# Kernel optimization log

Hardware: AMD Instinct MI355X
Metric: run time of the kernel (lower is better)

## Reference

```python
import jax, jax.numpy as jnp
import numpy as np

B, S, D, CH = 4, 2048, 1024, 64
MEM_LR, MEM_MOM, MEM_DECAY = 0.1, 0.9, 0.01
EPS = 1.1920929e-07  # torch RMSNorm default eps (float32 finfo eps)


def setup_inputs() -> dict:
    key = jax.random.key(0)
    ks = jax.random.split(key, 20)
    rn = lambda i, shape, s: jax.random.normal(ks[i], shape, dtype=jnp.float32) * s
    inp = {
        "x": jax.random.normal(ks[0], (B, S, D), dtype=jnp.float32),
        # archetypal metric M = I + small perturbation (near-identity, as in ArchetypalProjection)
        "Mmet": jnp.eye(D, dtype=jnp.float32)[None, :, :] + rn(1, (B, D, D), 0.02),
        # projections (bias-free, xavier-ish scale)
        "Wk": rn(2, (D, D), 0.02), "Wv": rn(3, (D, D), 0.02),
        "Wq": rn(4, (D, D), 0.02), "Wo": rn(5, (D, D), 0.02),
        # gate Linears (with bias) for decay / lr / momentum
        "Wgd": rn(6, (D, D), 0.02), "bgd": rn(7, (D,), 0.02),
        "Wgl": rn(8, (D, D), 0.02), "bgl": rn(9, (D,), 0.02),
        "Wgm": rn(10, (D, D), 0.02), "bgm": rn(11, (D,), 0.02),
        # RMSNorm gains
        "g_store": jnp.ones((D,), dtype=jnp.float32),
        "g_retr": jnp.ones((D,), dtype=jnp.float32),
        # memory MLP initial weights (depth=2, std=0.02)
        "W0": rn(12, (D, D), 0.02), "W1": rn(13, (D, D), 0.02),
    }
    return inp


def rmsnorm(x, g):
    return x * jax.lax.rsqrt(jnp.mean(x * x, axis=-1, keepdims=True) + EPS) * g


def l2norm(x):
    n = jnp.linalg.norm(x, axis=-1, keepdims=True)
    return x / jnp.maximum(n, 1e-12)


def mem_fwd(h, W0, W1):
    # 2-layer bias-free MLP with SiLU between layers (MemoryMLP, depth=2)
    return jax.nn.silu(h @ W0.T) @ W1.T


def forward(x, Mmet, Wk, Wv, Wq, Wo, Wgd, bgd, Wgl, bgl, Wgm, bgm, g_store, g_retr, W0, W1):
    Bs, Ss, Ds = x.shape
    pad = (-Ss) % CH
    xp = jnp.pad(x, ((0, 0), (0, pad), (0, 0))) if pad else x
    N = xp.shape[1] // CH

    # data-dependent per-chunk gates from chunk means -> batch-averaged scalars [N]
    cm = xp.reshape(Bs, N, CH, Ds).mean(axis=2)            # [B,N,D]
    alpha = jax.nn.sigmoid(cm @ Wgd.T + bgd).mean(-1).mean(0) * MEM_DECAY  # [N]
    theta = jax.nn.sigmoid(cm @ Wgl.T + bgl).mean(-1).mean(0) * MEM_LR     # [N]
    eta = jax.nn.sigmoid(cm @ Wgm.T + bgm).mean(-1).mean(0) * MEM_MOM      # [N]

    # store path: RMSNorm -> curved-space keys via archetypal metric
    xs = rmsnorm(xp, g_store)
    k = l2norm(jax.nn.silu(jnp.einsum('bsd,bde->bse', xs, Mmet) @ Wk.T))
    v = jax.nn.silu(xs @ Wv.T)
    # retrieve path
    q = l2norm(jax.nn.silu(rmsnorm(xp, g_retr) @ Wq.T))

    to_chunks = lambda t: t.reshape(Bs, N, CH, Ds).transpose(1, 0, 2, 3)  # [N,B,C,D]
    kc, vc, qc = to_chunks(k), to_chunks(v), to_chunks(q)

    def assoc_loss(params, kk, vv):
        return jnp.mean((mem_fwd(kk, *params) - vv) ** 2)

    grad_fn = jax.grad(assoc_loss)

    def step(carry, inp):
        W0c, W1c, S0, S1 = carry
        qt, kt, vt, a, th, et = inp
        r = mem_fwd(qt, W0c, W1c)                 # retrieve BEFORE update (causal)
        g0, g1 = grad_fn((W0c, W1c), kt, vt)      # surprise gradient
        S0n = et * S0 - th * g0                   # Eq. 14
        S1n = et * S1 - th * g1
        W0n = (1.0 - a) * W0c + S0n               # Eq. 13
        W1n = (1.0 - a) * W1c + S1n
        return (W0n, W1n, S0n, S1n), r

    init = (W0, W1, jnp.zeros_like(W0), jnp.zeros_like(W1))
    _, ret = jax.lax.scan(step, init, (qc, kc, vc, alpha, theta, eta))  # ret: [N,B,C,D]
    out = ret.transpose(1, 0, 2, 3).reshape(Bs, N * CH, Ds)[:, :Ss, :] @ Wo.T
    return out


def reference(x, Mmet, Wk, Wv, Wq, Wo, Wgd, bgd, Wgl, bgl, Wgm, bgm, g_store, g_retr, W0, W1):
    return forward(x, Mmet, Wk, Wv, Wq, Wo, Wgd, bgd, Wgl, bgl, Wgm, bgm, g_store, g_retr, W0, W1)
```

## Files before the change

### kernel.cpp

```cpp
#include <hip/hip_runtime.h>
#include <math.h>

static constexpr int B_ = 4, S_ = 2048, D_ = 1024, CH_ = 64, N_ = 32;
static constexpr float EPS_ = 1.1920929e-07f;
static constexpr float C2_  = 2.0f / 262144.0f;
static constexpr int GRID_ = 128;

typedef __attribute__((ext_vector_type(8))) short bf16x8;
typedef __attribute__((ext_vector_type(4))) short bf16x4;
typedef __attribute__((ext_vector_type(4))) float f32x4;

__device__ __forceinline__ float sigf(float x)  { return 1.f/(1.f+expf(-x)); }
__device__ __forceinline__ float siluf(float x) { return x/(1.f+expf(-x)); }
__device__ __forceinline__ float silugrad(float x){
  float s = 1.f/(1.f+expf(-x));
  return s*(1.f + x*(1.f-s));
}
__device__ __forceinline__ short f2b(float f){
  union{float f;unsigned u;}c; c.f=f;
  unsigned u=c.u;
  return (short)((u + 0x7fffu + ((u>>16)&1u)) >> 16);
}
__device__ __forceinline__ float b2f(short h){
  union{unsigned u;float f;}c; c.u=((unsigned)(unsigned short)h)<<16; return c.f;
}

template<int LPS>
__device__ __forceinline__ void wait_vm(int c){
  if (c <= 0)      asm volatile("s_waitcnt vmcnt(0)" ::: "memory");
  else if (c == 1) asm volatile("s_waitcnt vmcnt(%0)" :: "i"(LPS)   : "memory");
  else             asm volatile("s_waitcnt vmcnt(%0)" :: "i"(2*LPS) : "memory");
}

template<int MT, int NT, int DEPTH>
__device__ __forceinline__ void score(
    const short* __restrict__ A, const short* __restrict__ Bm,
    int K, int lda, int ldb, int bm0, int bn0, short* stg,
    f32x4 (&acc)[MT/32][NT/32])
{
  constexpr int MF = MT/32, NF = NT/32;
  constexpr int ACH = MT*8, BCH = NT*8, T = 256;
  constexpr int BUF = (MT+NT)*64;
  constexpr int LPS = (ACH+BCH)/T;
  const int tid = threadIdx.x, lane = tid & 63, w = tid >> 6;
  const int wm = w>>1, wn = w&1, lrow = lane & 15, lk8 = lane >> 4;

  #pragma unroll
  for (int i=0;i<MF;++i)
    #pragma unroll
    for (int j=0;j<NF;++j) acc[i][j] = (f32x4){0.f,0.f,0.f,0.f};

  auto stage = [&](int s){
    short* la = stg + (s & (DEPTH-1))*BUF;
    short* lb = la + MT*64;
    const int k0 = s*64;
    #pragma unroll
    for (int i=tid; i<ACH; i+=T){
      int row = i>>3, sc = (i&7) ^ (row&7);
      const short* src = A + (size_t)(bm0+row)*lda + k0 + (sc<<3);
      __builtin_amdgcn_global_load_lds(
        (const __attribute__((address_space(1))) void*)src,
        (__attribute__((address_space(3))) void*)(la + i*8), 16, 0, 0);
    }
    #pragma unroll
    for (int i=tid; i<BCH; i+=T){
      int row = i>>3, sc = (i&7) ^ (row&7);
      const short* src = Bm + (size_t)(bn0+row)*ldb + k0 + (sc<<3);
      __builtin_amdgcn_global_load_lds(
        (const __attribute__((address_space(1))) void*)src,
        (__attribute__((address_space(3))) void*)(lb + i*8), 16, 0, 0);
    }
  };

  const int nk = K >> 6;
  for (int s=0; s<DEPTH-1 && s<nk; ++s) stage(s);
  for (int ks=0; ks<nk; ++ks){
    int C = nk - ks; if (C > DEPTH-1) C = DEPTH-1;
    wait_vm<LPS>(C-1);
    __builtin_amdgcn_s_barrier();
    __builtin_amdgcn_sched_barrier(0);
    if (ks + DEPTH-1 < nk) stage(ks + DEPTH-1);
    short* la = stg + (ks & (DEPTH-1))*BUF;
    short* lb = la + MT*64;
    #pragma unroll
    for (int kk=0; kk<2; ++kk){
      bf16x8 af[MF], bfr[NF];
      #pragma unroll
      for (int mi=0;mi<MF;++mi){
        int row = wm*(MT/2) + mi*16 + lrow;
        int ch = row*8 + ((kk*4+lk8) ^ (row&7));
        af[mi] = *(const bf16x8*)(la + ch*8);
      }
      #pragma unroll
      for (int ni=0;ni<NF;++ni){
        int row = wn*(NT/2) + ni*16 + lrow;
        int ch = row*8 + ((kk*4+lk8) ^ (row&7));
        bfr[ni] = *(const bf16x8*)(lb + ch*8);
      }
      #pragma unroll
      for (int mi=0;mi<MF;++mi)
        #pragma unroll
        for (int ni=0;ni<NF;++ni)
          acc[mi][ni] = __builtin_amdgcn_mfma_f32_16x16x32_bf16(af[mi], bfr[ni], acc[mi][ni], 0,0,0);
    }
  }
}

template<int WMW, int WNW, int DEPTH, class Epi>
__device__ __forceinline__ void gemm_core(
    const short* __restrict__ A, const short* __restrict__ Bm,
    int K, int lda, int ldb, int bm0, int bn0, short* lds, Epi epi)
{
  constexpr int BK = 64, CPR = 8;
  constexpr int BMR = WMW*64, BNR = WNW*64, T = WMW*WNW*64;
  constexpr int ACH = BMR*CPR, BCH = BNR*CPR;
  constexpr int BUF = (BMR+BNR)*BK;
  constexpr int LPS = (ACH+BCH)/T;
  const int tid = threadIdx.x, lane = tid & 63, w = tid >> 6;
  const int wm = w / WNW, wn = w % WNW, lrow = lane & 15, lk8 = lane >> 4;

  f32x4 acc[4][4];
  #pragma unroll
  for (int i=0;i<4;++i)
    #pragma unroll
    for (int j=0;j<4;++j) acc[i][j] = (f32x4){0.f,0.f,0.f,0.f};

  auto stage = [&](int s){
    short* la = lds + (s & (DEPTH-1))*BUF;
    short* lb = la + BMR*BK;
    const int k0 = s*BK;
    #pragma unroll
    for (int i=tid; i<ACH; i+=T){
      int row = i>>3, sc = (i&7) ^ (row&7);
      const short* src = A + (size_t)(bm0+row)*lda + k0 + (sc<<3);
      __builtin_amdgcn_global_load_lds(
        (const __attribute__((address_space(1))) void*)src,
        (__attribute__((address_space(3))) void*)(la + i*8), 16, 0, 0);
    }
    #pragma unroll
    for (int i=tid; i<BCH; i+=T){
      int row = i>>3, sc = (i&7) ^ (row&7);
      const short* src = Bm + (size_t)(bn0+row)*ldb + k0 + (sc<<3);
      __builtin_amdgcn_global_load_lds(
        (const __attribute__((address_space(1))) void*)src,
        (__attribute__((address_space(3))) void*)(lb + i*8), 16, 0, 0);
    }
  };

  const int nk = K >> 6;
  for (int s=0; s<DEPTH-1 && s<nk; ++s) stage(s);
  for (int ks=0; ks<nk; ++ks){
    int C = nk - ks; if (C > DEPTH-1) C = DEPTH-1;
    wait_vm<LPS>(C-1);
    __builtin_amdgcn_s_barrier();
    __builtin_amdgcn_sched_barrier(0);
    if (ks + DEPTH-1 < nk) stage(ks + DEPTH-1);
    short* la = lds + (ks & (DEPTH-1))*BUF;
    short* lb = la + BMR*BK;
    #pragma unroll
    for (int kk=0; kk<2; ++kk){
      bf16x8 af[4], bfr[4];
      #pragma unroll
      for (int mi=0;mi<4;++mi){
        int row = wm*64 + mi*16 + lrow;
        int ch = row*8 + ((kk*4+lk8) ^ (row&7));
        af[mi] = *(const bf16x8*)(la + ch*8);
      }
      #pragma unroll
      for (int ni=0;ni<4;++ni){
        int row = wn*64 + ni*16 + lrow;
        int ch = row*8 + ((kk*4+lk8) ^ (row&7));
        bfr[ni] = *(const bf16x8*)(lb + ch*8);
      }
      #pragma unroll
      for (int mi=0;mi<4;++mi)
        #pragma unroll
        for (int ni=0;ni<4;++ni)
          acc[mi][ni] = __builtin_amdgcn_mfma_f32_16x16x32_bf16(af[mi], bfr[ni], acc[mi][ni], 0,0,0);
    }
  }
  #pragma unroll
  for (int mi=0;mi<4;++mi)
    #pragma unroll
    for (int ni=0;ni<4;++ni)
      epi(bm0 + wm*64 + mi*16 + lk8*4, bn0 + wn*64 + ni*16 + lrow, acc[mi][ni]);
}

struct EpiOut { float* C;
  __device__ void operator()(int r0,int c,f32x4 q) const {
    #pragma unroll
    for (int j=0;j<4;++j) C[(size_t)(r0+j)*D_+c]=q[j]; } };

struct EpiStoreBf { short* C;
  __device__ void operator()(int r0,int c,f32x4 q) const {
    #pragma unroll
    for (int j=0;j<4;++j) C[(size_t)(r0+j)*D_+c]=f2b(q[j]); } };

struct EpiBiasSig { float* C; const float* bias;
  __device__ void operator()(int r0,int c,f32x4 q) const {
    #pragma unroll
    for (int j=0;j<4;++j) C[(size_t)(r0+j)*D_+c] = sigf(q[j] + bias[c]); } };

struct EpiScat { short* dst; int part;
  __device__ void operator()(int r0,int c,f32x4 q) const {
    #pragma unroll
    for (int j=0;j<4;++j){
      int r = r0+j;
      int b = r >> 11, s = r & 2047, t = s >> 6, ch = s & 63;
      short sv = f2b(siluf(q[j]));
      if (part < 0) dst[((size_t)t*256 +             b*64 + ch)*D_ + c] = sv;
      else          dst[((size_t)t*512 + part*256 + b*64 + ch)*D_ + c] = sv;
    } } };

template<int WMW, int WNW, class Epi>
__global__ __launch_bounds__(WMW*WNW*64)
void mgemm(const short* __restrict__ A, const short* __restrict__ Bm,
           int K, int lda, int ldb, Epi epi){
  __shared__ __align__(16) short lds[2*(WMW+WNW)*64*64];
  gemm_core<WMW,WNW,2>(A, Bm, K, lda, ldb, blockIdx.y*WMW*64, blockIdx.x*WNW*64, lds, epi);
}

__device__ __forceinline__ void gsync(int* cnt, int target){
  asm volatile("s_waitcnt vmcnt(0) lgkmcnt(0)" ::: "memory");
  __syncthreads();
  if (threadIdx.x == 0){
    __builtin_amdgcn_fence(__ATOMIC_RELEASE, "agent");
    __hip_atomic_fetch_add(cnt, 1, __ATOMIC_RELAXED, __HIP_MEMORY_SCOPE_AGENT);
    while (__hip_atomic_load(cnt, __ATOMIC_RELAXED, __HIP_MEMORY_SCOPE_AGENT) < target)
      __builtin_amdgcn_s_sleep(4);
    __builtin_amdgcn_fence(__ATOMIC_ACQUIRE, "agent");
  }
  __syncthreads();
}

__global__ __launch_bounds__(256)
void scan_coop(const short* __restrict__ qk, const short* __restrict__ vbuf,
               const short* __restrict__ ktT, const float* __restrict__ gates,
               short* __restrict__ preout, short* __restrict__ sgT,
               short* __restrict__ abuf, short* __restrict__ akT,
               short* __restrict__ dpred, short* __restrict__ dpredT, short* __restrict__ dh1T,
               const float* __restrict__ W0f, const float* __restrict__ W1f,
               short* __restrict__ W0b, short* __restrict__ W1b,
               short* __restrict__ W1bT0, short* __restrict__ W1bT1,
               int* __restrict__ bar)
{
  __shared__ __align__(16) float wM[128*132];
  __shared__ __align__(16) short stg[32768];
  const int bid = blockIdx.x;
  const int tid = threadIdx.x, lane = tid & 63, w = tid >> 6;
  const int wm = w>>1, wn = w&1, lrow = lane & 15, lk8 = lane >> 4;
  int* cnt = bar;
  int ep = 0;

  const bool ownW1 = bid < 64;
  const int ob = ownW1 ? bid : bid - 64;
  const int obm = (ob>>3)<<7, obn = (ob&7)<<7;
  const float* Wsrc = ownW1 ? W1f : W0f;
  for (int i=tid; i<4096; i+=256){
    int cl = i>>5, r4 = (i&31)<<2;
    f32x4 v = *(const f32x4*)&Wsrc[(size_t)(obn+cl)*D_ + obm + r4];
    *(f32x4*)&wM[cl*132 + r4] = v;
  }
  f32x4 sReg[4][4];
  #pragma unroll
  for (int i=0;i<4;++i)
    #pragma unroll
    for (int j=0;j<4;++j) sReg[i][j] = (f32x4){0.f,0.f,0.f,0.f};
  __syncthreads();

  const int pbm0 = (bid>>4)<<6, pbn0 = (bid&15)<<6;

  for (int t=0; t<N_; ++t){
    const short* qkt = qk + (size_t)t*512*D_;
    const float al = gates[t], th = gates[N_+t], et = gates[2*N_+t];
    short* W1Tcur = (t&1) ? W1bT1 : W1bT0;
    short* W1Tnxt = (t&1) ? W1bT0 : W1bT1;

    {
      f32x4 acc[2][2];
      score<64,64,4>(qkt, W0b, 1024, 1024, 1024, pbm0, pbn0, stg, acc);
      #pragma unroll
      for (int mi=0;mi<2;++mi)
        #pragma unroll
        for (int ni=0;ni<2;++ni){
          int r0 = pbm0 + wm*32 + mi*16 + lk8*4;
          int c  = pbn0 + wn*32 + ni*16 + lrow;
          f32x4 q = acc[mi][ni];
          bf16x4 a4, g4;
          #pragma unroll
          for (int j=0;j<4;++j){
            a4[j] = f2b(siluf(q[j]));
            g4[j] = f2b(silugrad(q[j]));
            abuf[(size_t)(r0+j)*D_+c] = a4[j];
          }
          if (r0 >= 256){ int rr = r0-256;
            *(bf16x4*)&akT[(size_t)c*256+rr] = a4;
            *(bf16x4*)&sgT[(size_t)c*256+rr] = g4; }
        }
    }
    gsync(cnt, (++ep)*GRID_);

    {
      const short* vt = vbuf + (size_t)t*256*D_;
      f32x4 acc[2][2];
      score<64,64,4>(abuf, W1b, 1024, 1024, 1024, pbm0, pbn0, stg, acc);
      #pragma unroll
      for (int mi=0;mi<2;++mi)
        #pragma unroll
        for (int ni=0;ni<2;++ni){
          int r0 = pbm0 + wm*32 + mi*16 + lk8*4;
          int c  = pbn0 + wn*32 + ni*16 + lrow;
          f32x4 q = acc[mi][ni];
          if (r0 < 256){
            #pragma unroll
            for (int j=0;j<4;++j){ int r=r0+j, b=r>>6, ch=r&63;
              preout[((size_t)b*S_ + t*CH_ + ch)*D_ + c] = f2b(q[j]); }
          } else { int rr = r0-256;
            bf16x4 d4;
            #pragma unroll
            for (int j=0;j<4;++j){
              float dv = C2_*(q[j] - b2f(vt[(size_t)(rr+j)*D_+c]));
              d4[j] = f2b(dv);
              dpred[(size_t)(rr+j)*D_+c] = d4[j];
            }
            *(bf16x4*)&dpredT[(size_t)c*256+rr] = d4; }
        }
    }
    gsync(cnt, (++ep)*GRID_);
    if (t == N_-1) break;

    if (ownW1){
      f32x4 acc[4][4];
      score<128,128,2>(akT, dpredT, 256, 256, 256, obm, obn, stg, acc);
      #pragma unroll
      for (int mi=0;mi<4;++mi)
        #pragma unroll
        for (int ni=0;ni<4;++ni){
          int rl = wm*64 + mi*16 + lk8*4;
          int cl = wn*64 + ni*16 + lrow;
          f32x4 w4 = *(f32x4*)&wM[cl*132 + rl];
          f32x4 s4 = sReg[mi][ni];
          bf16x4 nb;
          #pragma unroll
          for (int j=0;j<4;++j){
            float sv = et*s4[j] - th*acc[mi][ni][j];
            s4[j] = sv;
            float wv = (1.f-al)*w4[j] + sv;
            w4[j] = wv; nb[j] = f2b(wv);
          }
          sReg[mi][ni] = s4;
          *(f32x4*)&wM[cl*132 + rl] = w4;
          int r0 = obm + rl, c = obn + cl;
          *(bf16x4*)&W1b[(size_t)c*D_ + r0] = nb;
          #pragma unroll
          for (int j=0;j<4;++j) W1Tnxt[(size_t)(r0+j)*D_ + c] = nb[j];
        }
    } else {
      int b = bid - 64;
      int bm0 = (b&15)<<6, bn0 = (b>>4)<<6;
      f32x4 acc[2][2];
      score<64,64,4>(W1Tcur, dpred, 1024, 1024, 1024, bm0, bn0, stg, acc);
      #pragma unroll
      for (int mi=0;mi<2;++mi)
        #pragma unroll
        for (int ni=0;ni<2;++ni){
          int r0 = bm0 + wm*32 + mi*16 + lk8*4;
          int c  = bn0 + wn*32 + ni*16 + lrow;
          #pragma unroll
          for (int j=0;j<4;++j){
            size_t i = (size_t)(r0+j)*256 + c;
            dh1T[i] = f2b(acc[mi][ni][j] * b2f(sgT[i]));
          }
        }
    }
    gsync(cnt, (++ep)*GRID_);

    if (!ownW1){
      f32x4 acc[4][4];
      score<128,128,2>(ktT + (size_t)t*D_*256, dh1T, 256, 256, 256, obm, obn, stg, acc);
      #pragma unroll
      for (int mi=0;mi<4;++mi)
        #pragma unroll
        for (int ni=0;ni<4;++ni){
          int rl = wm*64 + mi*16 + lk8*4;
          int cl = wn*64 + ni*16 + lrow;
          f32x4 w4 = *(f32x4*)&wM[cl*132 + rl];
          f32x4 s4 = sReg[mi][ni];
          bf16x4 nb;
          #pragma unroll
          for (int j=0;j<4;++j){
            float sv = et*s4[j] - th*acc[mi][ni][j];
            s4[j] = sv;
            float wv = (1.f-al)*w4[j] + sv;
            w4[j] = wv; nb[j] = f2b(wv);
          }
          sReg[mi][ni] = s4;
          *(f32x4*)&wM[cl*132 + rl] = w4;
          int r0 = obm + rl, c = obn + cl;
          *(bf16x4*)&W0b[(size_t)c*D_ + r0] = nb;
        }
    }
    gsync(cnt, (++ep)*GRID_);
  }
}

__device__ __forceinline__ float block_sum(float v){
  #pragma unroll
  for (int o=32;o>0;o>>=1) v += __shfl_down(v,o,64);
  __shared__ float sm4[4];
  int lane = threadIdx.x & 63, w = threadIdx.x >> 6;
  if (lane==0) sm4[w]=v;
  __syncthreads();
  float r = sm4[0]+sm4[1]+sm4[2]+sm4[3];
  __syncthreads();
  return r;
}

__global__ void conv_k(const float* __restrict__ s, short* __restrict__ d, int n4){
  int i = blockIdx.x*256 + threadIdx.x;
  if (i >= n4) return;
  float4 v = ((const float4*)s)[i];
  bf16x4 o = { f2b(v.x), f2b(v.y), f2b(v.z), f2b(v.w) };
  ((bf16x4*)d)[i] = o;
}

__global__ __launch_bounds__(256)
void transpose_bf_k(const short* __restrict__ in, short* __restrict__ out,
                    int R, int C, size_t ibs, size_t obs){
  __shared__ short t[64][68];
  const short* ip = in + blockIdx.z*ibs;
  short* op = out + blockIdx.z*obs;
  int r0 = blockIdx.y*64, c0 = blockIdx.x*64;
  for (int i=threadIdx.x; i<1024; i+=256){
    int r = i>>4, c4 = (i&15)*4;
    *(bf16x4*)&t[r][c4] = *(const bf16x4*)&ip[(size_t)(r0+r)*C + c0+c4];
  }
  __syncthreads();
  for (int i=threadIdx.x; i<1024; i+=256){
    int c = i>>4, r4 = (i&15)*4;
    bf16x4 v = { t[r4+0][c], t[r4+1][c], t[r4+2][c], t[r4+3][c] };
    *(bf16x4*)&op[(size_t)(c0+c)*R + r0+r4] = v;
  }
}

__global__ __launch_bounds__(256)
void transpose_f2b_k(const float* __restrict__ in, short* __restrict__ out,
                     int R, int C, size_t ibs, size_t obs){
  __shared__ short t[64][68];
  const float* ip = in + blockIdx.z*ibs;
  short* op = out + blockIdx.z*obs;
  int r0 = blockIdx.y*64, c0 = blockIdx.x*64;
  for (int i=threadIdx.x; i<1024; i+=256){
    int r = i>>4, c4 = (i&15)*4;
    float4 v = *(const float4*)&ip[(size_t)(r0+r)*C + c0+c4];
    t[r][c4+0]=f2b(v.x); t[r][c4+1]=f2b(v.y); t[r][c4+2]=f2b(v.z); t[r][c4+3]=f2b(v.w);
  }
  __syncthreads();
  for (int i=threadIdx.x; i<1024; i+=256){
    int c = i>>4, r4 = (i&15)*4;
    bf16x4 v = { t[r4+0][c], t[r4+1][c], t[r4+2][c], t[r4+3][c] };
    *(bf16x4*)&op[(size_t)(c0+c)*R + r0+r4] = v;
  }
}

__global__ void chunk_mean_k(const float* __restrict__ x, short* __restrict__ cm){
  int idx = blockIdx.x*256 + threadIdx.x;
  int d  = idx & (D_-1);
  int bn = idx >> 10;
  int b = bn >> 5, n = bn & 31;
  const float* p = x + ((size_t)b*S_ + n*CH_)*D_ + d;
  float s = 0.f;
  for (int ch=0; ch<CH_; ++ch) s += p[(size_t)ch*D_];
  cm[idx] = f2b(s * (1.f/CH_));
}

__global__ void gate_reduce_k(const float* __restrict__ Z, float* __restrict__ outp, float scale){
  int n = blockIdx.x;
  float s = 0.f;
  for (int b=0;b<B_;++b){
    const float* row = Z + (size_t)(b*N_+n)*D_;
    for (int j=threadIdx.x; j<D_; j+=256) s += row[j];
  }
  float tot = block_sum(s);
  if (threadIdx.x==0) outp[n] = scale * tot / (float)(B_*D_);
}

__global__ void rmsnorm2_k(const float* __restrict__ x, const float* __restrict__ gs,
                           const float* __restrict__ gr, short* __restrict__ xs, short* __restrict__ xr){
  size_t row = blockIdx.x;
  const float* xp = x + row*D_;
  float s = 0.f;
  for (int j=threadIdx.x;j<D_;j+=256){ float v=xp[j]; s+=v*v; }
  float tot = block_sum(s);
  float rinv = rsqrtf(tot/(float)D_ + EPS_);
  for (int j=threadIdx.x;j<D_;j+=256){
    float v = xp[j]*rinv;
    xs[row*D_+j] = f2b(v*gs[j]);
    xr[row*D_+j] = f2b(v*gr[j]);
  }
}

__global__ void l2norm_b(short* __restrict__ qk){
  size_t row = blockIdx.x;
  short* p = qk + row*D_;
  float s = 0.f;
  for (int j=threadIdx.x;j<D_;j+=256){ float v=b2f(p[j]); s+=v*v; }
  float tot = block_sum(s);
  float inv = 1.f / fmaxf(sqrtf(tot), 1e-12f);
  for (int j=threadIdx.x;j<D_;j+=256) p[j] = f2b(b2f(p[j])*inv);
}

__global__ void init_state_k(const float* __restrict__ W0, const float* __restrict__ W1,
                             short* __restrict__ W0b, short* __restrict__ W1b,
                             int* __restrict__ bar){
  size_t i = (size_t)blockIdx.x*256 + threadIdx.x;
  W0b[i]=f2b(W0[i]); W1b[i]=f2b(W1[i]);
  if (i==0){ bar[0]=0; bar[1]=0; }
}

extern "C" void kernel_launch(void* const* d_in, const int* in_sizes, int n_in,
                              void* d_out, int out_size, void* d_ws, size_t ws_size,
                              hipStream_t stream) {
  (void)in_sizes; (void)n_in; (void)out_size;
  const float* x    = (const float*)d_in[0];
  const float* Mmet = (const float*)d_in[1];
  const float* Wk   = (const float*)d_in[2];
  const float* Wv   = (const float*)d_in[3];
  const float* Wq   = (const float*)d_in[4];
  const float* Wo   = (const float*)d_in[5];
  const float* Wgd  = (const float*)d_in[6];
  const float* bgd  = (const float*)d_in[7];
  const float* Wgl  = (const float*)d_in[8];
  const float* bgl  = (const float*)d_in[9];
  const float* Wgm  = (const float*)d_in[10];
  const float* bgm  = (const float*)d_in[11];
  const float* g_store = (const float*)d_in[12];
  const float* g_retr  = (const float*)d_in[13];
  const float* W0   = (const float*)d_in[14];
  const float* W1   = (const float*)d_in[15];
  float* out = (float*)d_out;

  if (ws_size < 145000000ull) return;
  short* qk    = (short*)d_ws;
  short* vbuf  = qk    + 16777216;
  short* xs    = vbuf  + 8388608;
  short* xr    = xs    + 8388608;
  short* t1    = xr    + 8388608;
  short* cm    = t1    + 8388608;
  short* Wkb   = cm    + 131072;
  short* Wvb   = Wkb   + 1048576;
  short* Wqb   = Wvb   + 1048576;
  short* Wob   = Wqb   + 1048576;
  short* Wgdb  = Wob   + 1048576;
  short* Wglb  = Wgdb  + 1048576;
  short* Wgmb  = Wglb  + 1048576;
  short* MmetT = Wgmb  + 1048576;
  short* W0b   = MmetT + 4194304;
  short* W1b   = W0b   + 1048576;
  short* W1bT0 = W1b   + 1048576;
  short* W1bT1 = W1bT0 + 1048576;
  short* abuf  = W1bT1 + 1048576;
  short* akT   = abuf  + 524288;
  short* sgT   = akT   + 262144;
  short* dpred = sgT   + 262144;
  short* dpredT= dpred + 262144;
  short* dh1T  = dpredT+ 262144;
  float* Zg    = (float*)(dh1T + 262144);
  float* gates = Zg    + 131072;
  int*   bar   = (int*)(gates + 128);
  short* ktT   = xr;
  short* preout= t1;

  conv_k<<<1024,256,0,stream>>>(Wk,  Wkb,  262144);
  conv_k<<<1024,256,0,stream>>>(Wv,  Wvb,  262144);
  conv_k<<<1024,256,0,stream>>>(Wq,  Wqb,  262144);
  conv_k<<<1024,256,0,stream>>>(Wo,  Wob,  262144);
  conv_k<<<1024,256,0,stream>>>(Wgd, Wgdb, 262144);
  conv_k<<<1024,256,0,stream>>>(Wgl, Wglb, 262144);
  conv_k<<<1024,256,0,stream>>>(Wgm, Wgmb, 262144);
  transpose_f2b_k<<<dim3(16,16,4),256,0,stream>>>(Mmet, MmetT, 1024, 1024, 1048576, 1048576);
  init_state_k<<<4096,256,0,stream>>>(W0, W1, W0b, W1b, bar);
  transpose_bf_k<<<dim3(16,16,1),256,0,stream>>>(W1b, W1bT0, 1024, 1024, 0, 0);

  chunk_mean_k<<<512,256,0,stream>>>(x, cm);
  {
    dim3 g(8,1);
    mgemm<2,2,EpiBiasSig><<<g,256,0,stream>>>(cm, Wgdb, 1024,1024,1024, EpiBiasSig{Zg, bgd});
    gate_reduce_k<<<N_,256,0,stream>>>(Zg, gates + 0,    0.01f);
    mgemm<2,2,EpiBiasSig><<<g,256,0,stream>>>(cm, Wglb, 1024,1024,1024, EpiBiasSig{Zg, bgl});
    gate_reduce_k<<<N_,256,0,stream>>>(Zg, gates + N_,   0.1f);
    mgemm<2,2,EpiBiasSig><<<g,256,0,stream>>>(cm, Wgmb, 1024,1024,1024, EpiBiasSig{Zg, bgm});
    gate_reduce_k<<<N_,256,0,stream>>>(Zg, gates + 2*N_, 0.9f);
  }
  rmsnorm2_k<<<B_*S_,256,0,stream>>>(x, g_store, g_retr, xs, xr);
  for (int b=0;b<B_;++b)
    mgemm<2,2,EpiStoreBf><<<dim3(8,16),256,0,stream>>>(
      xs + (size_t)b*S_*D_, MmetT + (size_t)b*D_*D_, 1024,1024,1024,
      EpiStoreBf{t1 + (size_t)b*S_*D_});
  {
    dim3 g(8,64);
    mgemm<2,2,EpiScat><<<g,256,0,stream>>>(t1, Wkb, 1024,1024,1024, EpiScat{qk, 1});
    mgemm<2,2,EpiScat><<<g,256,0,stream>>>(xs, Wvb, 1024,1024,1024, EpiScat{vbuf,-1});
    mgemm<2,2,EpiScat><<<g,256,0,stream>>>(xr, Wqb, 1024,1024,1024, EpiScat{qk, 0});
  }
  l2norm_b<<<N_*512,256,0,stream>>>(qk);
  transpose_bf_k<<<dim3(16,4,32),256,0,stream>>>(qk + 256*1024, ktT, 256, 1024,
                                                 (size_t)512*1024, (size_t)1024*256);

  scan_coop<<<GRID_,256,0,stream>>>(qk, vbuf, ktT, gates, preout, sgT, abuf, akT,
                                    dpred, dpredT, dh1T, W0, W1,
                                    W0b, W1b, W1bT0, W1bT1, bar);

  mgemm<2,2,EpiOut><<<dim3(8,64),256,0,stream>>>(preout, Wob, 1024,1024,1024, EpiOut{out});
}
```

Measured before the change: 2.526 ms.

## Replace atomic-counter grid barrier with per-block flags and master release

Replaces the grid barrier built on a single atomic counter with per-block flag slots padded to 64 bytes. Block 0 polls all 128 flags with a wavefront-wide vote and then writes a release flag that every other block spins on. Release and acquire fences are skipped in the one phase where only the other block group writes data, and the final barrier of the last step is dropped. The aim is to cut atomic contention and barrier latency across the 32-step scan, at the cost of an extra hop through block 0 and more fragile memory-ordering reasoning.

```diff
diff --git a/kernel.cpp b/kernel.cpp
--- a/kernel.cpp
+++ b/kernel.cpp
@@ -220,15 +220,33 @@
   gemm_core<WMW,WNW,2>(A, Bm, K, lda, ldb, blockIdx.y*WMW*64, blockIdx.x*WNW*64, lds, epi);
 }
 
-__device__ __forceinline__ void gsync(int* cnt, int target){
+__device__ __forceinline__ void gsync(int* flags, int ep, bool do_rel, bool do_acq){
   asm volatile("s_waitcnt vmcnt(0) lgkmcnt(0)" ::: "memory");
   __syncthreads();
-  if (threadIdx.x == 0){
-    __builtin_amdgcn_fence(__ATOMIC_RELEASE, "agent");
-    __hip_atomic_fetch_add(cnt, 1, __ATOMIC_RELAXED, __HIP_MEMORY_SCOPE_AGENT);
-    while (__hip_atomic_load(cnt, __ATOMIC_RELAXED, __HIP_MEMORY_SCOPE_AGENT) < target)
-      __builtin_amdgcn_s_sleep(4);
-    __builtin_amdgcn_fence(__ATOMIC_ACQUIRE, "agent");
+  const int bid = blockIdx.x, tid = threadIdx.x;
+  int* rel = flags + 2048;
+  if (tid == 0){
+    if (do_rel) __builtin_amdgcn_fence(__ATOMIC_RELEASE, "agent");
+    __hip_atomic_store(&flags[bid*16], ep, __ATOMIC_RELAXED, __HIP_MEMORY_SCOPE_SYSTEM);
+  }
+  if (bid == 0){
+    if (tid < 64){
+      for(;;){
+        int a = __hip_atomic_load(&flags[tid*16],      __ATOMIC_RELAXED, __HIP_MEMORY_SCOPE_SYSTEM);
+        int b = __hip_atomic_load(&flags[(tid+64)*16], __ATOMIC_RELAXED, __HIP_MEMORY_SCOPE_SYSTEM);
+        if (__all(a >= ep && b >= ep)) break;
+        __builtin_amdgcn_s_sleep(1);
+      }
+    }
+    __syncthreads();
+    if (tid == 0)
+      __hip_atomic_store(rel, ep, __ATOMIC_RELAXED, __HIP_MEMORY_SCOPE_SYSTEM);
+  }
+  if (tid == 0){
+    if (bid != 0)
+      while (__hip_atomic_load(rel, __ATOMIC_RELAXED, __HIP_MEMORY_SCOPE_SYSTEM) < ep)
+        __builtin_amdgcn_s_sleep(1);
+    if (do_acq) __builtin_amdgcn_fence(__ATOMIC_ACQUIRE, "agent");
   }
   __syncthreads();
 }
@@ -249,7 +267,6 @@
   const int bid = blockIdx.x;
   const int tid = threadIdx.x, lane = tid & 63, w = tid >> 6;
   const int wm = w>>1, wn = w&1, lrow = lane & 15, lk8 = lane >> 4;
-  int* cnt = bar;
   int ep = 0;
 
   const bool ownW1 = bid < 64;
@@ -298,7 +315,7 @@
             *(bf16x4*)&sgT[(size_t)c*256+rr] = g4; }
         }
     }
-    gsync(cnt, (++ep)*GRID_);
+    gsync(bar, ++ep, true, true);
 
     {
       const short* vt = vbuf + (size_t)t*256*D_;
@@ -326,8 +343,8 @@
             *(bf16x4*)&dpredT[(size_t)c*256+rr] = d4; }
         }
     }
-    gsync(cnt, (++ep)*GRID_);
     if (t == N_-1) break;
+    gsync(bar, ++ep, true, true);
 
     if (ownW1){
       f32x4 acc[4][4];
@@ -373,7 +390,7 @@
           }
         }
     }
-    gsync(cnt, (++ep)*GRID_);
+    gsync(bar, ++ep, !ownW1, !ownW1);
 
     if (!ownW1){
       f32x4 acc[4][4];
@@ -400,7 +417,7 @@
           *(bf16x4*)&W0b[(size_t)c*D_ + r0] = nb;
         }
     }
-    gsync(cnt, (++ep)*GRID_);
+    gsync(bar, ++ep, true, true);
   }
 }
 
@@ -515,7 +532,7 @@
                              int* __restrict__ bar){
   size_t i = (size_t)blockIdx.x*256 + threadIdx.x;
   W0b[i]=f2b(W0[i]); W1b[i]=f2b(W1[i]);
-  if (i==0){ bar[0]=0; bar[1]=0; }
+  if (i < 4096) bar[i] = 0;
 }
 
 extern "C" void kernel_launch(void* const* d_in, const int* in_sizes, int n_in,
```

Result: faster. 2.213 ms (-12.4%).
